# Kernel optimization log

Measured on AMD Instinct MI355X. Metric: run time of the kernel, lower is better.

Reference implementation:

```python
import jax, jax.numpy as jnp
import numpy as np

B, D, SLOTS, TOPK, CODE, ANCH = 8192, 64, 32, 3, 128, 32
BETA = 0.25  # vq_commitment_beta


def _clinear(zr, zi, Wr, Wi, br, bi):
    # ComplexLinear: real = Wr(zr)-Wi(zi), imag = Wi(zr)+Wr(zi); each nn.Linear carries its own bias
    return (zr @ Wr + br) - (zi @ Wi + bi), (zr @ Wi + bi) + (zi @ Wr + br)


def _layernorm(x, g, b, eps=1e-6):
    m = x.mean(-1, keepdims=True)
    v = ((x - m) ** 2).mean(-1, keepdims=True)  # biased var, as torch LayerNorm
    return (x - m) / jnp.sqrt(v + eps) * g + b


def setup_inputs() -> dict:
    key = jax.random.key(0)
    ks = jax.random.split(key, 16)
    f = jax.random.normal
    s = 0.05
    rng_init = 1.0 / np.sqrt(D)
    return dict(
        curr_r=f(ks[0], (B, D)), curr_i=f(ks[1], (B, D)),
        mem_r=f(ks[2], (B, SLOTS, D)), mem_i=f(ks[3], (B, SLOTS, D)),
        codebook=jax.random.uniform(ks[4], (CODE, 2 * D), minval=-rng_init, maxval=rng_init),
        qkv_Wr=f(ks[5], (3, D, D)) * s, qkv_Wi=f(ks[6], (3, D, D)) * s,
        qkv_br=jnp.zeros((3, D)), qkv_bi=jnp.zeros((3, D)),
        quad_Wr=f(ks[7], (D, D)) * s, quad_Wi=f(ks[8], (D, D)) * s,
        quad_br=jnp.zeros((D,)), quad_bi=jnp.zeros((D,)),
        sens_Wr=f(ks[9], (D, D)) * s, sens_Wi=f(ks[10], (D, D)) * s,
        sens_br=jnp.zeros((D,)), sens_bi=jnp.zeros((D,)),
        vis_palette=f(ks[11], (ANCH, 2 * D)), aud_palette=f(ks[12], (ANCH, 2 * D)),
        gate_W=f(ks[13], (2 * D, 1)) * s, gate_b=jnp.zeros((1,)),
        addr_W=f(ks[14], (2 * D, SLOTS)) * s, addr_b=jnp.zeros((SLOTS,)),
        ln_gamma_r=jnp.ones((D,)), ln_beta_r=jnp.zeros((D,)),
        ln_gamma_i=jnp.ones((D,)), ln_beta_i=jnp.zeros((D,)),
    )


def reference(curr_r, curr_i, mem_r, mem_i, codebook,
              qkv_Wr, qkv_Wi, qkv_br, qkv_bi,
              quad_Wr, quad_Wi, quad_br, quad_bi,
              sens_Wr, sens_Wi, sens_br, sens_bi,
              vis_palette, aud_palette,
              gate_W, gate_b, addr_W, addr_b,
              ln_gamma_r, ln_beta_r, ln_gamma_i, ln_beta_i):
    sg = jax.lax.stop_gradient
    z_flat = jnp.concatenate([curr_r, curr_i], -1)  # [B,2D]

    # ---- EMA_VQ (eval path): argmin codebook lookup + straight-through ----
    d = (z_flat ** 2).sum(1, keepdims=True) + (codebook ** 2).sum(1) - 2.0 * z_flat @ codebook.T
    d = jnp.maximum(d, 0.0)
    indices = jnp.argmin(d, -1)                      # [B]
    z_q = codebook[indices]                          # [B,2D]
    vq_loss = BETA * ((sg(z_q) - z_flat) ** 2).mean(-1)
    z_q = z_flat + sg(z_q - z_flat)
    probs = jnp.zeros((CODE,), z_flat.dtype).at[indices].add(1.0) / B
    norm_entropy = -(probs * jnp.log(probs + 1e-10)).sum() / np.log(CODE)
    vq_r, vq_i = z_q[..., :D], z_q[..., D:]

    # ---- HermitianGating ----
    qr, qi = _clinear(curr_r, curr_i, qkv_Wr[0], qkv_Wi[0], qkv_br[0], qkv_bi[0])
    kr, ki = _clinear(curr_r, curr_i, qkv_Wr[1], qkv_Wi[1], qkv_br[1], qkv_bi[1])
    vr, vi = _clinear(curr_r, curr_i, qkv_Wr[2], qkv_Wi[2], qkv_br[2], qkv_bi[2])
    gate = jax.nn.sigmoid((qr * kr + qi * ki).sum(-1, keepdims=True))
    g_r, g_i = vr * gate, vi * gate

    # ---- AssociativeMemory: softmax read + topk scatter write ----
    sim = jnp.einsum('bsd,bd->bs', mem_r, curr_r) + jnp.einsum('bsd,bd->bs', mem_i, curr_i)
    sim = sim - sg(sim.max(-1, keepdims=True))
    attn = jax.nn.softmax(sim, -1)
    read_r = jnp.einsum('bs,bsd->bd', attn, mem_r)
    read_i = jnp.einsum('bs,bsd->bd', attn, mem_i)
    write_gate = jax.nn.sigmoid(z_flat @ gate_W + gate_b)[:, :, None]  # [B,1,1]
    logits = z_flat @ addr_W + addr_b
    logits = logits - sg(logits.max(-1, keepdims=True))
    ww = jax.nn.softmax(logits, -1)                  # [B,SLOTS]
    slot_entropy = (-(ww * jnp.log(ww + 1e-10)).sum(-1)).mean()
    top_vals, top_idx = jax.lax.top_k(ww, TOPK)
    sparse = jnp.zeros_like(ww).at[jnp.arange(B)[:, None], top_idx].set(top_vals)
    sparse = sparse / (sparse.sum(-1, keepdims=True) + 1e-6)
    eff = write_gate * sparse[..., None]             # [B,SLOTS,1]
    nm_r = jnp.tanh(mem_r + eff * (curr_r[:, None, :] - mem_r))
    nm_i = jnp.tanh(mem_i + eff * (curr_i[:, None, :] - mem_i))
    nm_r = _layernorm(nm_r, ln_gamma_r, ln_beta_r)
    nm_i = _layernorm(nm_i, ln_gamma_i, ln_beta_i)

    # ---- SubmodalityAnchorModule ----
    s_r, s_i = _clinear(curr_r, curr_i, sens_Wr, sens_Wi, sens_br, sens_bi)
    sflat = jnp.concatenate([s_r, s_i], -1)

    def attend(pal):
        sc = sflat @ pal.T
        sc = sc - sg(sc.max(-1, keepdims=True))
        return jax.nn.softmax(sc, -1) @ pal

    vis = attend(vis_palette)
    aud = attend(aud_palette)
    exp_r = vis[..., :D] - aud[..., D:]   # vis_c + i*aud_c
    exp_i = vis[..., D:] + aud[..., :D]

    # ---- QuadratureModule: multiply by i ----
    zr, zi = _clinear(curr_r, curr_i, quad_Wr, quad_Wi, quad_br, quad_bi)
    q_r, q_i = -zi, zr

    combined = jnp.concatenate(
        [vq_r, vq_i, g_r, g_i, read_r, read_i, exp_r, exp_i, q_r, q_i,
         nm_r.reshape(B, -1), nm_i.reshape(B, -1)], -1)  # [B, 10*D + 2*SLOTS*D]
    return combined, vq_loss, indices, slot_entropy, norm_entropy
```

## Files before the change

### kernel.cpp

```cpp
#include <hip/hip_runtime.h>
#include <hip/hip_bf16.h>


#define NROWS 8
#define RSTRIDE 4736

static constexpr size_t OFF_VQLOSS = 38797312UL;
static constexpr size_t OFF_IDX    = 38805504UL;
static constexpr size_t OFF_SENT   = 38813696UL;
static constexpr size_t OFF_NENT   = 38813697UL;

struct Params {
  const float* curr_r; const float* curr_i;
  const float* mem_r;  const float* mem_i;
  const float* codebook;
  const float* qkv_Wr; const float* qkv_Wi; const float* qkv_br; const float* qkv_bi;
  const float* quad_Wr; const float* quad_Wi; const float* quad_br; const float* quad_bi;
  const float* sens_Wr; const float* sens_Wi; const float* sens_br; const float* sens_bi;
  const float* vis_pal; const float* aud_pal;
  const float* gate_W; const float* gate_b;
  const float* addr_W; const float* addr_b;
  const float* ln_gr; const float* ln_br; const float* ln_gi; const float* ln_bi;
  float* out;
  int* hist;
  float* rowent;
};

__device__ __forceinline__ float ftanh(float x) {
  const float e = __expf(2.0f * x);
  return 1.0f - 2.0f / (e + 1.0f);
}
__device__ __forceinline__ float fsigm(float x) {
  return 1.0f / (1.0f + __expf(-x));
}

union __align__(16) SharedU {
  struct {
    float zr[64], zi[64];
    float s_qr[64], s_qi[64], s_kr[64], s_ki[64], s_vr[64], s_vi[64];
    float sfl[128];
    float s_sp[4][4][64];
    float lp[4][32];
    float s_eff[32];
    float s_sim[32], s_attn[32];
    float s_rr[4][8][8], s_ri[4][8][8];
    float s_pv[4][32], s_pa[4][32];
    float s_pvp[32], s_pap[32];
    float s_vo[128], s_ao[128];
    float s_wg, s_gate;
  } r;
  struct {
    float s_zr[NROWS][64], s_zi[NROWS][64];
    double s_cbn[128];
    double s_dall4[4][256];
    float s_vqls[NROWS];
    int s_idx[NROWS];
  } v;
};

__global__ __launch_bounds__(256) void main_kernel(Params P) {
  __shared__ SharedU u;
  const int t = threadIdx.x;
  const int lane = t & 63;
  const int wv = t >> 6;

  if (blockIdx.x < 1024) {
    const int bid = blockIdx.x;
    {
      const float* cr = P.curr_r + (size_t)bid * (NROWS * 64);
      const float* ci = P.curr_i + (size_t)bid * (NROWS * 64);
      float* zr = &u.v.s_zr[0][0];
      float* zi = &u.v.s_zi[0][0];
      for (int i = t; i < NROWS * 64; i += 256) { zr[i] = cr[i]; zi[i] = ci[i]; }
    }
    {
      const float* cb = P.codebook + (t & 127) * 128 + (t >> 7) * 64;
      double a = 0.0;
      for (int d = 0; d < 64; ++d) { double w = (double)cb[d]; a = fma(w, w, a); }
      __syncthreads();
      ((double*)&u.v.s_dall4[0][0])[t] = a;
      __syncthreads();
      if (t < 128) u.v.s_cbn[t] = ((double*)&u.v.s_dall4[0][0])[t]
                                 + ((double*)&u.v.s_dall4[0][0])[t + 128];
      __syncthreads();
    }
    {
      const int c = t & 127, h = t >> 7;
      const float* cb = P.codebook + c * 128 + h * 64;
      const float (*zb)[64] = h ? u.v.s_zi : u.v.s_zr;
      #pragma unroll 1
      for (int p = 0; p < 2; ++p) {
        double acc[4];
        #pragma unroll
        for (int rr = 0; rr < 4; ++rr) acc[rr] = 0.0;
        for (int d = 0; d < 64; ++d) {
          const double w = (double)cb[d];
          #pragma unroll
          for (int rr = 0; rr < 4; ++rr) acc[rr] = fma(w, (double)zb[p * 4 + rr][d], acc[rr]);
        }
        #pragma unroll
        for (int rr = 0; rr < 4; ++rr) u.v.s_dall4[rr][h * 128 + c] = acc[rr];
        __syncthreads();
        {
          const int r = p * 4 + wv;
          const double d0 = u.v.s_cbn[lane]      - 2.0 * (u.v.s_dall4[wv][lane]      + u.v.s_dall4[wv][128 + lane]);
          const double d1 = u.v.s_cbn[lane + 64] - 2.0 * (u.v.s_dall4[wv][64 + lane] + u.v.s_dall4[wv][192 + lane]);
          double sv = d0; int si = lane;
          if (d1 < sv) { sv = d1; si = lane + 64; }
          #pragma unroll
          for (int m = 1; m <= 32; m <<= 1) {
            double ov = __shfl_xor(sv, m);
            int oi = __shfl_xor(si, m);
            if (ov < sv || (ov == sv && oi < si)) { sv = ov; si = oi; }
          }
          if (lane == 0) { u.v.s_idx[r] = si; atomicAdd(&P.hist[si], 1); }
        }
        __syncthreads();
      }
    }
    {
      #pragma unroll
      for (int rr = 0; rr < 2; ++rr) {
        const int r = wv * 2 + rr;
        const float* cb = P.codebook + (size_t)u.v.s_idx[r] * 128;
        float d0_ = cb[lane] - u.v.s_zr[r][lane];
        float d1_ = cb[64 + lane] - u.v.s_zi[r][lane];
        float v = d0_ * d0_ + d1_ * d1_;
        #pragma unroll
        for (int m = 1; m <= 32; m <<= 1) v += __shfl_xor(v, m);
        if (lane == 0) u.v.s_vqls[r] = 0.25f * v * (1.0f / 128.0f);
      }
    }
    __syncthreads();
    {
      const int j = t & 63, g = t >> 6;
      #pragma unroll
      for (int rr = 0; rr < 4; ++rr) {
        const int r = (g >> 1) * 4 + rr;
        float* orow = P.out + ((size_t)bid * NROWS + r) * RSTRIDE;
        const float* cb = P.codebook + (size_t)u.v.s_idx[r] * 128;
        if ((g & 1) == 0) {
          float z = u.v.s_zr[r][j];
          orow[j] = z + (cb[j] - z);
        } else {
          float z = u.v.s_zi[r][j];
          orow[64 + j] = z + (cb[64 + j] - z);
        }
      }
    }
    if (t < NROWS) {
      P.out[OFF_VQLOSS + (size_t)bid * NROWS + t] = u.v.s_vqls[t];
      P.out[OFF_IDX + (size_t)bid * NROWS + t] = (float)u.v.s_idx[t];
    }
    return;
  }

  const int b = blockIdx.x - 1024;
  const size_t bb = (size_t)b;
  const int s = t >> 3, k = t & 7, d0 = k * 8;
  const float* mrp = P.mem_r + ((bb * 32 + s) * 64 + d0);
  const float* mip = P.mem_i + ((bb * 32 + s) * 64 + d0);
  float4 a0 = *(const float4*)mrp, a1 = *(const float4*)(mrp + 4);
  float4 b0 = *(const float4*)mip, b1 = *(const float4*)(mip + 4);
  float mr[8] = {a0.x, a0.y, a0.z, a0.w, a1.x, a1.y, a1.z, a1.w};
  float mi[8] = {b0.x, b0.y, b0.z, b0.w, b1.x, b1.y, b1.z, b1.w};

  if (t < 64)       u.r.zr[t]      = P.curr_r[bb * 64 + t];
  else if (t < 128) u.r.zi[t - 64] = P.curr_i[bb * 64 + (t - 64)];
  __syncthreads();

  float* orow = P.out + bb * RSTRIDE;

  {
    const int j = lane, cl = wv;
    const float *Wr, *Wi, *br_, *bi_;
    if      (cl == 0) { Wr = P.qkv_Wr;        Wi = P.qkv_Wi;        br_ = P.qkv_br;       bi_ = P.qkv_bi;       }
    else if (cl == 1) { Wr = P.qkv_Wr + 4096; Wi = P.qkv_Wi + 4096; br_ = P.qkv_br + 64;  bi_ = P.qkv_bi + 64;  }
    else if (cl == 2) { Wr = P.qkv_Wr + 8192; Wi = P.qkv_Wi + 8192; br_ = P.qkv_br + 128; bi_ = P.qkv_bi + 128; }
    else              { Wr = P.quad_Wr;       Wi = P.quad_Wi;       br_ = P.quad_br;      bi_ = P.quad_bi;      }
    float aRR = 0.f, aRI = 0.f, aIR = 0.f, aII = 0.f;
    for (int d = 0; d < 64; ++d) {
      const float xr = u.r.zr[d], xi = u.r.zi[d];
      const float wr = Wr[d * 64 + j], wi = Wi[d * 64 + j];
      aRR += xr * wr; aRI += xr * wi; aIR += xi * wr; aII += xi * wi;
    }
    const float oR = (aRR + br_[j]) - (aII + bi_[j]);
    const float oI = (aRI + bi_[j]) + (aIR + br_[j]);
    if      (cl == 0) { u.r.s_qr[j] = oR; u.r.s_qi[j] = oI; }
    else if (cl == 1) { u.r.s_kr[j] = oR; u.r.s_ki[j] = oI; }
    else if (cl == 2) { u.r.s_vr[j] = oR; u.r.s_vi[j] = oI; }
    else              { orow[512 + j] = -oI; orow[576 + j] = oR; }
    float bRR = 0.f, bRI = 0.f, bIR = 0.f, bII = 0.f;
    for (int dd = 0; dd < 16; ++dd) {
      const int d = wv * 16 + dd;
      const float xr = u.r.zr[d], xi = u.r.zi[d];
      const float wr = P.sens_Wr[d * 64 + j], wi = P.sens_Wi[d * 64 + j];
      bRR += xr * wr; bRI += xr * wi; bIR += xi * wr; bII += xi * wi;
    }
    u.r.s_sp[wv][0][j] = bRR; u.r.s_sp[wv][1][j] = bRI;
    u.r.s_sp[wv][2][j] = bIR; u.r.s_sp[wv][3][j] = bII;
  }
  __syncthreads();

  {
    float sp = 0.f;
    #pragma unroll
    for (int x = 0; x < 8; ++x) sp += mr[x] * u.r.zr[d0 + x] + mi[x] * u.r.zi[d0 + x];
    sp += __shfl_xor(sp, 1); sp += __shfl_xor(sp, 2); sp += __shfl_xor(sp, 4);
    if (k == 0) u.r.s_sim[s] = sp;
  }
  if (t < 128) {
    const int q = t >> 5, l = t & 31;
    const float* zz = (q < 2) ? u.r.zr : u.r.zi;
    const int zb = (q & 1) * 32;
    float a = 0.f;
    for (int i = 0; i < 32; ++i) a += zz[zb + i] * P.addr_W[(q * 32 + i) * 32 + l];
    u.r.lp[q][l] = a;
  } else if (t < 192) {
    const int j = t - 128;
    float tw = u.r.zr[j] * P.gate_W[j] + u.r.zi[j] * P.gate_W[64 + j];
    #pragma unroll
    for (int m = 1; m <= 32; m <<= 1) tw += __shfl_xor(tw, m);
    if (j == 0) u.r.s_wg = tw;
  } else {
    const int j = t - 192;
    float g = u.r.s_qr[j] * u.r.s_kr[j] + u.r.s_qi[j] * u.r.s_ki[j];
    #pragma unroll
    for (int m = 1; m <= 32; m <<= 1) g += __shfl_xor(g, m);
    if (j == 0) u.r.s_gate = fsigm(g);
  }
  __syncthreads();

  if (t < 32) {
    float v = u.r.s_sim[t];
    float mx = v;
    #pragma unroll
    for (int m = 16; m >= 1; m >>= 1) mx = fmaxf(mx, __shfl_xor(mx, m));
    float e = __expf(v - mx);
    float sm = e;
    #pragma unroll
    for (int m = 16; m >= 1; m >>= 1) sm += __shfl_xor(sm, m);
    u.r.s_attn[t] = e / sm;
  } else if (t >= 64 && t < 96) {
    const int l = t - 64;
    float lg = u.r.lp[0][l] + u.r.lp[1][l] + u.r.lp[2][l] + u.r.lp[3][l] + P.addr_b[l];
    float mx = lg;
    #pragma unroll
    for (int m = 16; m >= 1; m >>= 1) mx = fmaxf(mx, __shfl_xor(mx, m));
    float e = __expf(lg - mx);
    float sm = e;
    #pragma unroll
    for (int m = 16; m >= 1; m >>= 1) sm += __shfl_xor(sm, m);
    const float w = e / sm;
    float es = -(w * __logf(w + 1e-10f));
    #pragma unroll
    for (int m = 16; m >= 1; m >>= 1) es += __shfl_xor(es, m);
    if (l == 0) P.rowent[b] = es;
    const float myw = w;
    bool picked = false;
    float val = w; int idx = l;
    float sumtop = 0.f;
    #pragma unroll
    for (int it = 0; it < 3; ++it) {
      float v2 = val; int i2 = idx;
      #pragma unroll
      for (int m = 16; m >= 1; m >>= 1) {
        float ov = __shfl_xor(v2, m); int oi = __shfl_xor(i2, m);
        if (ov > v2 || (ov == v2 && oi < i2)) { v2 = ov; i2 = oi; }
      }
      sumtop += v2;
      if (l == i2) { picked = true; val = -1e30f; }
    }
    const float wgate = fsigm(u.r.s_wg + P.gate_b[0]);
    u.r.s_eff[l] = picked ? wgate * (myw / (sumtop + 1e-6f)) : 0.f;
  } else if (t >= 128 && t < 192) {
    const int j = t - 128;
    const float aRR = u.r.s_sp[0][0][j] + u.r.s_sp[1][0][j] + u.r.s_sp[2][0][j] + u.r.s_sp[3][0][j];
    const float aRI = u.r.s_sp[0][1][j] + u.r.s_sp[1][1][j] + u.r.s_sp[2][1][j] + u.r.s_sp[3][1][j];
    const float aIR = u.r.s_sp[0][2][j] + u.r.s_sp[1][2][j] + u.r.s_sp[2][2][j] + u.r.s_sp[3][2][j];
    const float aII = u.r.s_sp[0][3][j] + u.r.s_sp[1][3][j] + u.r.s_sp[2][3][j] + u.r.s_sp[3][3][j];
    const float oR = (aRR + P.sens_br[j]) - (aII + P.sens_bi[j]);
    const float oI = (aRI + P.sens_bi[j]) + (aIR + P.sens_br[j]);
    u.r.sfl[j] = oR; u.r.sfl[64 + j] = oI;
  }
  __syncthreads();

  const float aw = u.r.s_attn[s];
  {
    float pr[8], pi[8];
    #pragma unroll
    for (int x = 0; x < 8; ++x) { pr[x] = aw * mr[x]; pi[x] = aw * mi[x]; }
    #pragma unroll
    for (int m = 8; m <= 32; m <<= 1) {
      #pragma unroll
      for (int x = 0; x < 8; ++x) { pr[x] += __shfl_xor(pr[x], m); pi[x] += __shfl_xor(pi[x], m); }
    }
    if (lane < 8) {
      #pragma unroll
      for (int x = 0; x < 8; ++x) { u.r.s_rr[wv][lane][x] = pr[x]; u.r.s_ri[wv][lane][x] = pi[x]; }
    }
  }
  {
    const float eff = u.r.s_eff[s];
    float nr[8], ni[8];
    #pragma unroll
    for (int x = 0; x < 8; ++x) {
      nr[x] = ftanh(mr[x] + eff * (u.r.zr[d0 + x] - mr[x]));
      ni[x] = ftanh(mi[x] + eff * (u.r.zi[d0 + x] - mi[x]));
    }
    float sR = 0.f, sI = 0.f;
    #pragma unroll
    for (int x = 0; x < 8; ++x) { sR += nr[x]; sI += ni[x]; }
    sR += __shfl_xor(sR, 1); sR += __shfl_xor(sR, 2); sR += __shfl_xor(sR, 4);
    sI += __shfl_xor(sI, 1); sI += __shfl_xor(sI, 2); sI += __shfl_xor(sI, 4);
    const float mR = sR * (1.f / 64.f), mI = sI * (1.f / 64.f);
    float vR = 0.f, vI = 0.f;
    #pragma unroll
    for (int x = 0; x < 8; ++x) {
      const float dr = nr[x] - mR; vR += dr * dr;
      const float di = ni[x] - mI; vI += di * di;
    }
    vR += __shfl_xor(vR, 1); vR += __shfl_xor(vR, 2); vR += __shfl_xor(vR, 4);
    vI += __shfl_xor(vI, 1); vI += __shfl_xor(vI, 2); vI += __shfl_xor(vI, 4);
    const float invR = 1.f / sqrtf(vR * (1.f / 64.f) + 1e-6f);
    const float invI = 1.f / sqrtf(vI * (1.f / 64.f) + 1e-6f);
    float oR[8], oI[8];
    #pragma unroll
    for (int x = 0; x < 8; ++x) {
      const int d = d0 + x;
      oR[x] = (nr[x] - mR) * invR * P.ln_gr[d] + P.ln_br[d];
      oI[x] = (ni[x] - mI) * invI * P.ln_gi[d] + P.ln_bi[d];
    }
    *(float4*)&orow[640 + s * 64 + d0]      = make_float4(oR[0], oR[1], oR[2], oR[3]);
    *(float4*)&orow[640 + s * 64 + d0 + 4]  = make_float4(oR[4], oR[5], oR[6], oR[7]);
    *(float4*)&orow[2688 + s * 64 + d0]     = make_float4(oI[0], oI[1], oI[2], oI[3]);
    *(float4*)&orow[2688 + s * 64 + d0 + 4] = make_float4(oI[4], oI[5], oI[6], oI[7]);
  }
  if (t < 128) {
    const int a = t & 31, q = t >> 5;
    float sc = 0.f;
    for (int x = q * 32; x < q * 32 + 32; ++x) sc += u.r.sfl[x] * P.vis_pal[a * 128 + x];
    u.r.s_pv[q][a] = sc;
  } else {
    const int tt = t - 128, a = tt & 31, q = tt >> 5;
    float sc = 0.f;
    for (int x = q * 32; x < q * 32 + 32; ++x) sc += u.r.sfl[x] * P.aud_pal[a * 128 + x];
    u.r.s_pa[q][a] = sc;
  }
  __syncthreads();

  if (t < 64) {
    const int kk = t >> 3, xx = t & 7;
    const float rv = u.r.s_rr[0][kk][xx] + u.r.s_rr[1][kk][xx] + u.r.s_rr[2][kk][xx] + u.r.s_rr[3][kk][xx];
    const float iv = u.r.s_ri[0][kk][xx] + u.r.s_ri[1][kk][xx] + u.r.s_ri[2][kk][xx] + u.r.s_ri[3][kk][xx];
    orow[256 + t] = rv;
    orow[320 + t] = iv;
  } else if (t >= 128 && t < 160) {
    const int a = t - 128;
    float sc = u.r.s_pv[0][a] + u.r.s_pv[1][a] + u.r.s_pv[2][a] + u.r.s_pv[3][a];
    float mx = sc;
    #pragma unroll
    for (int m = 16; m >= 1; m >>= 1) mx = fmaxf(mx, __shfl_xor(mx, m));
    float e = __expf(sc - mx);
    float sm = e;
    #pragma unroll
    for (int m = 16; m >= 1; m >>= 1) sm += __shfl_xor(sm, m);
    u.r.s_pvp[a] = e / sm;
  } else if (t >= 192 && t < 224) {
    const int a = t - 192;
    float sc = u.r.s_pa[0][a] + u.r.s_pa[1][a] + u.r.s_pa[2][a] + u.r.s_pa[3][a];
    float mx = sc;
    #pragma unroll
    for (int m = 16; m >= 1; m >>= 1) mx = fmaxf(mx, __shfl_xor(mx, m));
    float e = __expf(sc - mx);
    float sm = e;
    #pragma unroll
    for (int m = 16; m >= 1; m >>= 1) sm += __shfl_xor(sm, m);
    u.r.s_pap[a] = e / sm;
  }
  __syncthreads();

  if (t < 128) {
    float v = 0.f;
    for (int a = 0; a < 32; ++a) v += u.r.s_pvp[a] * P.vis_pal[a * 128 + t];
    u.r.s_vo[t] = v;
  } else {
    const int j = t - 128;
    float v = 0.f;
    for (int a = 0; a < 32; ++a) v += u.r.s_pap[a] * P.aud_pal[a * 128 + j];
    u.r.s_ao[j] = v;
  }
  if (t < 64)       orow[128 + t] = u.r.s_vr[t] * u.r.s_gate;
  else if (t < 128) orow[192 + (t - 64)] = u.r.s_vi[t - 64] * u.r.s_gate;
  __syncthreads();

  if (t < 64)       orow[384 + t] = u.r.s_vo[t] - u.r.s_ao[64 + t];
  else if (t < 128) orow[448 + (t - 64)] = u.r.s_vo[t] + u.r.s_ao[t - 64];
}

__global__ __launch_bounds__(256) void finalize_k(const int* hist, const float* rowent,
                                                  float* out) {
  const int t = threadIdx.x;
  __shared__ float red[256];
  float se = 0.f;
  for (int i = t; i < 8192; i += 256) se += rowent[i];
  red[t] = se;
  __syncthreads();
  for (int off = 128; off >= 1; off >>= 1) {
    if (t < off) red[t] += red[t + off];
    __syncthreads();
  }
  if (t == 0) out[OFF_SENT] = red[0] / 8192.0f;
  __syncthreads();
  float ne = 0.f;
  if (t < 128) {
    const float pp = (float)hist[t] / 8192.0f;
    ne = -(pp * logf(pp + 1e-10f));
  }
  red[t] = ne;
  __syncthreads();
  for (int off = 128; off >= 1; off >>= 1) {
    if (t < off) red[t] += red[t + off];
    __syncthreads();
  }
  if (t == 0) out[OFF_NENT] = red[0] / logf(128.0f);
}

extern "C" void kernel_launch(void* const* d_in, const int* in_sizes, int n_in,
                              void* d_out, int out_size, void* d_ws, size_t ws_size,
                              hipStream_t stream) {
  (void)in_sizes; (void)n_in; (void)out_size; (void)ws_size;
  Params P;
  P.curr_r   = (const float*)d_in[0];
  P.curr_i   = (const float*)d_in[1];
  P.mem_r    = (const float*)d_in[2];
  P.mem_i    = (const float*)d_in[3];
  P.codebook = (const float*)d_in[4];
  P.qkv_Wr   = (const float*)d_in[5];
  P.qkv_Wi   = (const float*)d_in[6];
  P.qkv_br   = (const float*)d_in[7];
  P.qkv_bi   = (const float*)d_in[8];
  P.quad_Wr  = (const float*)d_in[9];
  P.quad_Wi  = (const float*)d_in[10];
  P.quad_br  = (const float*)d_in[11];
  P.quad_bi  = (const float*)d_in[12];
  P.sens_Wr  = (const float*)d_in[13];
  P.sens_Wi  = (const float*)d_in[14];
  P.sens_br  = (const float*)d_in[15];
  P.sens_bi  = (const float*)d_in[16];
  P.vis_pal  = (const float*)d_in[17];
  P.aud_pal  = (const float*)d_in[18];
  P.gate_W   = (const float*)d_in[19];
  P.gate_b   = (const float*)d_in[20];
  P.addr_W   = (const float*)d_in[21];
  P.addr_b   = (const float*)d_in[22];
  P.ln_gr    = (const float*)d_in[23];
  P.ln_br    = (const float*)d_in[24];
  P.ln_gi    = (const float*)d_in[25];
  P.ln_bi    = (const float*)d_in[26];
  P.out = (float*)d_out;
  P.hist = (int*)d_ws;
  P.rowent = (float*)((char*)d_ws + 512);

  hipMemsetAsync(d_ws, 0, 512, stream);
  main_kernel<<<dim3(1024 + 8192), dim3(256), 0, stream>>>(P);
  finalize_k<<<dim3(1), dim3(256), 0, stream>>>(P.hist, P.rowent, (float*)d_out);
}
```

Before: 234.4 us.

## Process four batch rows per block with register prefetch of next row

Each per-row block now loops over four consecutive batch rows, and the grid shrinks from 8192 row blocks to 2048. While computing the current row, it prefetches the next row's memory slots and current vector into registers, so global load latency overlaps with compute. Weight reads from cache are shared across rows. In exchange each block runs longer, there are fewer blocks to spread over the GPU, an extra barrier is added per row, and register pressure rises.

```diff
diff --git a/kernel.cpp b/kernel.cpp
--- a/kernel.cpp
+++ b/kernel.cpp
@@ -155,247 +155,278 @@
     return;
   }
 
-  const int b = blockIdx.x - 1024;
-  const size_t bb = (size_t)b;
+  const int base = (blockIdx.x - 1024) * 4;
   const int s = t >> 3, k = t & 7, d0 = k * 8;
-  const float* mrp = P.mem_r + ((bb * 32 + s) * 64 + d0);
-  const float* mip = P.mem_i + ((bb * 32 + s) * 64 + d0);
-  float4 a0 = *(const float4*)mrp, a1 = *(const float4*)(mrp + 4);
-  float4 b0 = *(const float4*)mip, b1 = *(const float4*)(mip + 4);
-  float mr[8] = {a0.x, a0.y, a0.z, a0.w, a1.x, a1.y, a1.z, a1.w};
-  float mi[8] = {b0.x, b0.y, b0.z, b0.w, b1.x, b1.y, b1.z, b1.w};
-
-  if (t < 64)       u.r.zr[t]      = P.curr_r[bb * 64 + t];
-  else if (t < 128) u.r.zi[t - 64] = P.curr_i[bb * 64 + (t - 64)];
+
+  float mrC[8], miC[8], mrN[8], miN[8];
+  {
+    const size_t bb0 = (size_t)base;
+    const float* mrp = P.mem_r + ((bb0 * 32 + s) * 64 + d0);
+    const float* mip = P.mem_i + ((bb0 * 32 + s) * 64 + d0);
+    float4 a0 = *(const float4*)mrp, a1 = *(const float4*)(mrp + 4);
+    float4 b0 = *(const float4*)mip, b1 = *(const float4*)(mip + 4);
+    mrC[0]=a0.x; mrC[1]=a0.y; mrC[2]=a0.z; mrC[3]=a0.w; mrC[4]=a1.x; mrC[5]=a1.y; mrC[6]=a1.z; mrC[7]=a1.w;
+    miC[0]=b0.x; miC[1]=b0.y; miC[2]=b0.z; miC[3]=b0.w; miC[4]=b1.x; miC[5]=b1.y; miC[6]=b1.z; miC[7]=b1.w;
+    if (t < 64)       u.r.zr[t]      = P.curr_r[bb0 * 64 + t];
+    else if (t < 128) u.r.zi[t - 64] = P.curr_i[bb0 * 64 + (t - 64)];
+  }
   __syncthreads();
 
-  float* orow = P.out + bb * RSTRIDE;
-
-  {
-    const int j = lane, cl = wv;
-    const float *Wr, *Wi, *br_, *bi_;
-    if      (cl == 0) { Wr = P.qkv_Wr;        Wi = P.qkv_Wi;        br_ = P.qkv_br;       bi_ = P.qkv_bi;       }
-    else if (cl == 1) { Wr = P.qkv_Wr + 4096; Wi = P.qkv_Wi + 4096; br_ = P.qkv_br + 64;  bi_ = P.qkv_bi + 64;  }
-    else if (cl == 2) { Wr = P.qkv_Wr + 8192; Wi = P.qkv_Wi + 8192; br_ = P.qkv_br + 128; bi_ = P.qkv_bi + 128; }
-    else              { Wr = P.quad_Wr;       Wi = P.quad_Wi;       br_ = P.quad_br;      bi_ = P.quad_bi;      }
-    float aRR = 0.f, aRI = 0.f, aIR = 0.f, aII = 0.f;
-    for (int d = 0; d < 64; ++d) {
-      const float xr = u.r.zr[d], xi = u.r.zi[d];
-      const float wr = Wr[d * 64 + j], wi = Wi[d * 64 + j];
-      aRR += xr * wr; aRI += xr * wi; aIR += xi * wr; aII += xi * wi;
-    }
-    const float oR = (aRR + br_[j]) - (aII + bi_[j]);
-    const float oI = (aRI + bi_[j]) + (aIR + br_[j]);
-    if      (cl == 0) { u.r.s_qr[j] = oR; u.r.s_qi[j] = oI; }
-    else if (cl == 1) { u.r.s_kr[j] = oR; u.r.s_ki[j] = oI; }
-    else if (cl == 2) { u.r.s_vr[j] = oR; u.r.s_vi[j] = oI; }
-    else              { orow[512 + j] = -oI; orow[576 + j] = oR; }
-    float bRR = 0.f, bRI = 0.f, bIR = 0.f, bII = 0.f;
-    for (int dd = 0; dd < 16; ++dd) {
-      const int d = wv * 16 + dd;
-      const float xr = u.r.zr[d], xi = u.r.zi[d];
-      const float wr = P.sens_Wr[d * 64 + j], wi = P.sens_Wi[d * 64 + j];
-      bRR += xr * wr; bRI += xr * wi; bIR += xi * wr; bII += xi * wi;
-    }
-    u.r.s_sp[wv][0][j] = bRR; u.r.s_sp[wv][1][j] = bRI;
-    u.r.s_sp[wv][2][j] = bIR; u.r.s_sp[wv][3][j] = bII;
-  }
-  __syncthreads();
-
-  {
-    float sp = 0.f;
-    #pragma unroll
-    for (int x = 0; x < 8; ++x) sp += mr[x] * u.r.zr[d0 + x] + mi[x] * u.r.zi[d0 + x];
-    sp += __shfl_xor(sp, 1); sp += __shfl_xor(sp, 2); sp += __shfl_xor(sp, 4);
-    if (k == 0) u.r.s_sim[s] = sp;
-  }
-  if (t < 128) {
-    const int q = t >> 5, l = t & 31;
-    const float* zz = (q < 2) ? u.r.zr : u.r.zi;
-    const int zb = (q & 1) * 32;
-    float a = 0.f;
-    for (int i = 0; i < 32; ++i) a += zz[zb + i] * P.addr_W[(q * 32 + i) * 32 + l];
-    u.r.lp[q][l] = a;
-  } else if (t < 192) {
-    const int j = t - 128;
-    float tw = u.r.zr[j] * P.gate_W[j] + u.r.zi[j] * P.gate_W[64 + j];
-    #pragma unroll
-    for (int m = 1; m <= 32; m <<= 1) tw += __shfl_xor(tw, m);
-    if (j == 0) u.r.s_wg = tw;
-  } else {
-    const int j = t - 192;
-    float g = u.r.s_qr[j] * u.r.s_kr[j] + u.r.s_qi[j] * u.r.s_ki[j];
-    #pragma unroll
-    for (int m = 1; m <= 32; m <<= 1) g += __shfl_xor(g, m);
-    if (j == 0) u.r.s_gate = fsigm(g);
-  }
-  __syncthreads();
-
-  if (t < 32) {
-    float v = u.r.s_sim[t];
-    float mx = v;
-    #pragma unroll
-    for (int m = 16; m >= 1; m >>= 1) mx = fmaxf(mx, __shfl_xor(mx, m));
-    float e = __expf(v - mx);
-    float sm = e;
-    #pragma unroll
-    for (int m = 16; m >= 1; m >>= 1) sm += __shfl_xor(sm, m);
-    u.r.s_attn[t] = e / sm;
-  } else if (t >= 64 && t < 96) {
-    const int l = t - 64;
-    float lg = u.r.lp[0][l] + u.r.lp[1][l] + u.r.lp[2][l] + u.r.lp[3][l] + P.addr_b[l];
-    float mx = lg;
-    #pragma unroll
-    for (int m = 16; m >= 1; m >>= 1) mx = fmaxf(mx, __shfl_xor(mx, m));
-    float e = __expf(lg - mx);
-    float sm = e;
-    #pragma unroll
-    for (int m = 16; m >= 1; m >>= 1) sm += __shfl_xor(sm, m);
-    const float w = e / sm;
-    float es = -(w * __logf(w + 1e-10f));
-    #pragma unroll
-    for (int m = 16; m >= 1; m >>= 1) es += __shfl_xor(es, m);
-    if (l == 0) P.rowent[b] = es;
-    const float myw = w;
-    bool picked = false;
-    float val = w; int idx = l;
-    float sumtop = 0.f;
-    #pragma unroll
-    for (int it = 0; it < 3; ++it) {
-      float v2 = val; int i2 = idx;
-      #pragma unroll
-      for (int m = 16; m >= 1; m >>= 1) {
-        float ov = __shfl_xor(v2, m); int oi = __shfl_xor(i2, m);
-        if (ov > v2 || (ov == v2 && oi < i2)) { v2 = ov; i2 = oi; }
-      }
-      sumtop += v2;
-      if (l == i2) { picked = true; val = -1e30f; }
-    }
-    const float wgate = fsigm(u.r.s_wg + P.gate_b[0]);
-    u.r.s_eff[l] = picked ? wgate * (myw / (sumtop + 1e-6f)) : 0.f;
-  } else if (t >= 128 && t < 192) {
-    const int j = t - 128;
-    const float aRR = u.r.s_sp[0][0][j] + u.r.s_sp[1][0][j] + u.r.s_sp[2][0][j] + u.r.s_sp[3][0][j];
-    const float aRI = u.r.s_sp[0][1][j] + u.r.s_sp[1][1][j] + u.r.s_sp[2][1][j] + u.r.s_sp[3][1][j];
-    const float aIR = u.r.s_sp[0][2][j] + u.r.s_sp[1][2][j] + u.r.s_sp[2][2][j] + u.r.s_sp[3][2][j];
-    const float aII = u.r.s_sp[0][3][j] + u.r.s_sp[1][3][j] + u.r.s_sp[2][3][j] + u.r.s_sp[3][3][j];
-    const float oR = (aRR + P.sens_br[j]) - (aII + P.sens_bi[j]);
-    const float oI = (aRI + P.sens_bi[j]) + (aIR + P.sens_br[j]);
-    u.r.sfl[j] = oR; u.r.sfl[64 + j] = oI;
-  }
-  __syncthreads();
-
-  const float aw = u.r.s_attn[s];
-  {
-    float pr[8], pi[8];
-    #pragma unroll
-    for (int x = 0; x < 8; ++x) { pr[x] = aw * mr[x]; pi[x] = aw * mi[x]; }
-    #pragma unroll
-    for (int m = 8; m <= 32; m <<= 1) {
-      #pragma unroll
-      for (int x = 0; x < 8; ++x) { pr[x] += __shfl_xor(pr[x], m); pi[x] += __shfl_xor(pi[x], m); }
-    }
-    if (lane < 8) {
-      #pragma unroll
-      for (int x = 0; x < 8; ++x) { u.r.s_rr[wv][lane][x] = pr[x]; u.r.s_ri[wv][lane][x] = pi[x]; }
-    }
-  }
-  {
-    const float eff = u.r.s_eff[s];
-    float nr[8], ni[8];
-    #pragma unroll
-    for (int x = 0; x < 8; ++x) {
-      nr[x] = ftanh(mr[x] + eff * (u.r.zr[d0 + x] - mr[x]));
-      ni[x] = ftanh(mi[x] + eff * (u.r.zi[d0 + x] - mi[x]));
-    }
-    float sR = 0.f, sI = 0.f;
-    #pragma unroll
-    for (int x = 0; x < 8; ++x) { sR += nr[x]; sI += ni[x]; }
-    sR += __shfl_xor(sR, 1); sR += __shfl_xor(sR, 2); sR += __shfl_xor(sR, 4);
-    sI += __shfl_xor(sI, 1); sI += __shfl_xor(sI, 2); sI += __shfl_xor(sI, 4);
-    const float mR = sR * (1.f / 64.f), mI = sI * (1.f / 64.f);
-    float vR = 0.f, vI = 0.f;
-    #pragma unroll
-    for (int x = 0; x < 8; ++x) {
-      const float dr = nr[x] - mR; vR += dr * dr;
-      const float di = ni[x] - mI; vI += di * di;
-    }
-    vR += __shfl_xor(vR, 1); vR += __shfl_xor(vR, 2); vR += __shfl_xor(vR, 4);
-    vI += __shfl_xor(vI, 1); vI += __shfl_xor(vI, 2); vI += __shfl_xor(vI, 4);
-    const float invR = 1.f / sqrtf(vR * (1.f / 64.f) + 1e-6f);
-    const float invI = 1.f / sqrtf(vI * (1.f / 64.f) + 1e-6f);
-    float oR[8], oI[8];
-    #pragma unroll
-    for (int x = 0; x < 8; ++x) {
-      const int d = d0 + x;
-      oR[x] = (nr[x] - mR) * invR * P.ln_gr[d] + P.ln_br[d];
-      oI[x] = (ni[x] - mI) * invI * P.ln_gi[d] + P.ln_bi[d];
-    }
-    *(float4*)&orow[640 + s * 64 + d0]      = make_float4(oR[0], oR[1], oR[2], oR[3]);
-    *(float4*)&orow[640 + s * 64 + d0 + 4]  = make_float4(oR[4], oR[5], oR[6], oR[7]);
-    *(float4*)&orow[2688 + s * 64 + d0]     = make_float4(oI[0], oI[1], oI[2], oI[3]);
-    *(float4*)&orow[2688 + s * 64 + d0 + 4] = make_float4(oI[4], oI[5], oI[6], oI[7]);
-  }
-  if (t < 128) {
-    const int a = t & 31, q = t >> 5;
-    float sc = 0.f;
-    for (int x = q * 32; x < q * 32 + 32; ++x) sc += u.r.sfl[x] * P.vis_pal[a * 128 + x];
-    u.r.s_pv[q][a] = sc;
-  } else {
-    const int tt = t - 128, a = tt & 31, q = tt >> 5;
-    float sc = 0.f;
-    for (int x = q * 32; x < q * 32 + 32; ++x) sc += u.r.sfl[x] * P.aud_pal[a * 128 + x];
-    u.r.s_pa[q][a] = sc;
-  }
-  __syncthreads();
-
-  if (t < 64) {
-    const int kk = t >> 3, xx = t & 7;
-    const float rv = u.r.s_rr[0][kk][xx] + u.r.s_rr[1][kk][xx] + u.r.s_rr[2][kk][xx] + u.r.s_rr[3][kk][xx];
-    const float iv = u.r.s_ri[0][kk][xx] + u.r.s_ri[1][kk][xx] + u.r.s_ri[2][kk][xx] + u.r.s_ri[3][kk][xx];
-    orow[256 + t] = rv;
-    orow[320 + t] = iv;
-  } else if (t >= 128 && t < 160) {
-    const int a = t - 128;
-    float sc = u.r.s_pv[0][a] + u.r.s_pv[1][a] + u.r.s_pv[2][a] + u.r.s_pv[3][a];
-    float mx = sc;
-    #pragma unroll
-    for (int m = 16; m >= 1; m >>= 1) mx = fmaxf(mx, __shfl_xor(mx, m));
-    float e = __expf(sc - mx);
-    float sm = e;
-    #pragma unroll
-    for (int m = 16; m >= 1; m >>= 1) sm += __shfl_xor(sm, m);
-    u.r.s_pvp[a] = e / sm;
-  } else if (t >= 192 && t < 224) {
-    const int a = t - 192;
-    float sc = u.r.s_pa[0][a] + u.r.s_pa[1][a] + u.r.s_pa[2][a] + u.r.s_pa[3][a];
-    float mx = sc;
-    #pragma unroll
-    for (int m = 16; m >= 1; m >>= 1) mx = fmaxf(mx, __shfl_xor(mx, m));
-    float e = __expf(sc - mx);
-    float sm = e;
-    #pragma unroll
-    for (int m = 16; m >= 1; m >>= 1) sm += __shfl_xor(sm, m);
-    u.r.s_pap[a] = e / sm;
-  }
-  __syncthreads();
-
-  if (t < 128) {
-    float v = 0.f;
-    for (int a = 0; a < 32; ++a) v += u.r.s_pvp[a] * P.vis_pal[a * 128 + t];
-    u.r.s_vo[t] = v;
-  } else {
-    const int j = t - 128;
-    float v = 0.f;
-    for (int a = 0; a < 32; ++a) v += u.r.s_pap[a] * P.aud_pal[a * 128 + j];
-    u.r.s_ao[j] = v;
-  }
-  if (t < 64)       orow[128 + t] = u.r.s_vr[t] * u.r.s_gate;
-  else if (t < 128) orow[192 + (t - 64)] = u.r.s_vi[t - 64] * u.r.s_gate;
-  __syncthreads();
-
-  if (t < 64)       orow[384 + t] = u.r.s_vo[t] - u.r.s_ao[64 + t];
-  else if (t < 128) orow[448 + (t - 64)] = u.r.s_vo[t] + u.r.s_ao[t - 64];
+  #pragma unroll
+  for (int rr = 0; rr < 4; ++rr) {
+    const int b = base + rr;
+    const size_t bb = (size_t)b;
+    float* orow = P.out + bb * RSTRIDE;
+
+    float zn = 0.f;
+    if (rr < 3) {
+      const size_t bn = bb + 1;
+      const float* mrp = P.mem_r + ((bn * 32 + s) * 64 + d0);
+      const float* mip = P.mem_i + ((bn * 32 + s) * 64 + d0);
+      float4 a0 = *(const float4*)mrp, a1 = *(const float4*)(mrp + 4);
+      float4 b0 = *(const float4*)mip, b1 = *(const float4*)(mip + 4);
+      mrN[0]=a0.x; mrN[1]=a0.y; mrN[2]=a0.z; mrN[3]=a0.w; mrN[4]=a1.x; mrN[5]=a1.y; mrN[6]=a1.z; mrN[7]=a1.w;
+      miN[0]=b0.x; miN[1]=b0.y; miN[2]=b0.z; miN[3]=b0.w; miN[4]=b1.x; miN[5]=b1.y; miN[6]=b1.z; miN[7]=b1.w;
+      if (t < 64)       zn = P.curr_r[bn * 64 + t];
+      else if (t < 128) zn = P.curr_i[bn * 64 + (t - 64)];
+    }
+
+    {
+      const int j = lane, cl = wv;
+      const float *Wr, *Wi, *br_, *bi_;
+      if      (cl == 0) { Wr = P.qkv_Wr;        Wi = P.qkv_Wi;        br_ = P.qkv_br;       bi_ = P.qkv_bi;       }
+      else if (cl == 1) { Wr = P.qkv_Wr + 4096; Wi = P.qkv_Wi + 4096; br_ = P.qkv_br + 64;  bi_ = P.qkv_bi + 64;  }
+      else if (cl == 2) { Wr = P.qkv_Wr + 8192; Wi = P.qkv_Wi + 8192; br_ = P.qkv_br + 128; bi_ = P.qkv_bi + 128; }
+      else              { Wr = P.quad_Wr;       Wi = P.quad_Wi;       br_ = P.quad_br;      bi_ = P.quad_bi;      }
+      float aRR = 0.f, aRI = 0.f, aIR = 0.f, aII = 0.f;
+      for (int d = 0; d < 64; ++d) {
+        const float xr = u.r.zr[d], xi = u.r.zi[d];
+        const float wr = Wr[d * 64 + j], wi = Wi[d * 64 + j];
+        aRR += xr * wr; aRI += xr * wi; aIR += xi * wr; aII += xi * wi;
+      }
+      const float oR = (aRR + br_[j]) - (aII + bi_[j]);
+      const float oI = (aRI + bi_[j]) + (aIR + br_[j]);
+      if      (cl == 0) { u.r.s_qr[j] = oR; u.r.s_qi[j] = oI; }
+      else if (cl == 1) { u.r.s_kr[j] = oR; u.r.s_ki[j] = oI; }
+      else if (cl == 2) { u.r.s_vr[j] = oR; u.r.s_vi[j] = oI; }
+      else              { orow[512 + j] = -oI; orow[576 + j] = oR; }
+      float bRR = 0.f, bRI = 0.f, bIR = 0.f, bII = 0.f;
+      for (int dd = 0; dd < 16; ++dd) {
+        const int d = wv * 16 + dd;
+        const float xr = u.r.zr[d], xi = u.r.zi[d];
+        const float wr = P.sens_Wr[d * 64 + j], wi = P.sens_Wi[d * 64 + j];
+        bRR += xr * wr; bRI += xr * wi; bIR += xi * wr; bII += xi * wi;
+      }
+      u.r.s_sp[wv][0][j] = bRR; u.r.s_sp[wv][1][j] = bRI;
+      u.r.s_sp[wv][2][j] = bIR; u.r.s_sp[wv][3][j] = bII;
+    }
+    __syncthreads();
+
+    {
+      float sp = 0.f;
+      #pragma unroll
+      for (int x = 0; x < 8; ++x) sp += mrC[x] * u.r.zr[d0 + x] + miC[x] * u.r.zi[d0 + x];
+      sp += __shfl_xor(sp, 1); sp += __shfl_xor(sp, 2); sp += __shfl_xor(sp, 4);
+      if (k == 0) u.r.s_sim[s] = sp;
+    }
+    if (t < 128) {
+      const int q = t >> 5, l = t & 31;
+      const float* zz = (q < 2) ? u.r.zr : u.r.zi;
+      const int zb = (q & 1) * 32;
+      float a = 0.f;
+      for (int i = 0; i < 32; ++i) a += zz[zb + i] * P.addr_W[(q * 32 + i) * 32 + l];
+      u.r.lp[q][l] = a;
+    } else if (t < 192) {
+      const int j = t - 128;
+      float tw = u.r.zr[j] * P.gate_W[j] + u.r.zi[j] * P.gate_W[64 + j];
+      #pragma unroll
+      for (int m = 1; m <= 32; m <<= 1) tw += __shfl_xor(tw, m);
+      if (j == 0) u.r.s_wg = tw;
+    } else {
+      const int j = t - 192;
+      float g = u.r.s_qr[j] * u.r.s_kr[j] + u.r.s_qi[j] * u.r.s_ki[j];
+      #pragma unroll
+      for (int m = 1; m <= 32; m <<= 1) g += __shfl_xor(g, m);
+      if (j == 0) u.r.s_gate = fsigm(g);
+    }
+    __syncthreads();
+
+    if (t < 32) {
+      float v = u.r.s_sim[t];
+      float mx = v;
+      #pragma unroll
+      for (int m = 16; m >= 1; m >>= 1) mx = fmaxf(mx, __shfl_xor(mx, m));
+      float e = __expf(v - mx);
+      float sm = e;
+      #pragma unroll
+      for (int m = 16; m >= 1; m >>= 1) sm += __shfl_xor(sm, m);
+      u.r.s_attn[t] = e / sm;
+    } else if (t >= 64 && t < 96) {
+      const int l = t - 64;
+      float lg = u.r.lp[0][l] + u.r.lp[1][l] + u.r.lp[2][l] + u.r.lp[3][l] + P.addr_b[l];
+      float mx = lg;
+      #pragma unroll
+      for (int m = 16; m >= 1; m >>= 1) mx = fmaxf(mx, __shfl_xor(mx, m));
+      float e = __expf(lg - mx);
+      float sm = e;
+      #pragma unroll
+      for (int m = 16; m >= 1; m >>= 1) sm += __shfl_xor(sm, m);
+      const float w = e / sm;
+      float es = -(w * __logf(w + 1e-10f));
+      #pragma unroll
+      for (int m = 16; m >= 1; m >>= 1) es += __shfl_xor(es, m);
+      if (l == 0) P.rowent[b] = es;
+      const float myw = w;
+      bool picked = false;
+      float val = w; int idx = l;
+      float sumtop = 0.f;
+      #pragma unroll
+      for (int it = 0; it < 3; ++it) {
+        float v2 = val; int i2 = idx;
+        #pragma unroll
+        for (int m = 16; m >= 1; m >>= 1) {
+          float ov = __shfl_xor(v2, m); int oi = __shfl_xor(i2, m);
+          if (ov > v2 || (ov == v2 && oi < i2)) { v2 = ov; i2 = oi; }
+        }
+        sumtop += v2;
+        if (l == i2) { picked = true; val = -1e30f; }
+      }
+      const float wgate = fsigm(u.r.s_wg + P.gate_b[0]);
+      u.r.s_eff[l] = picked ? wgate * (myw / (sumtop + 1e-6f)) : 0.f;
+    } else if (t >= 128 && t < 192) {
+      const int j = t - 128;
+      const float aRR = u.r.s_sp[0][0][j] + u.r.s_sp[1][0][j] + u.r.s_sp[2][0][j] + u.r.s_sp[3][0][j];
+      const float aRI = u.r.s_sp[0][1][j] + u.r.s_sp[1][1][j] + u.r.s_sp[2][1][j] + u.r.s_sp[3][1][j];
+      const float aIR = u.r.s_sp[0][2][j] + u.r.s_sp[1][2][j] + u.r.s_sp[2][2][j] + u.r.s_sp[3][2][j];
+      const float aII = u.r.s_sp[0][3][j] + u.r.s_sp[1][3][j] + u.r.s_sp[2][3][j] + u.r.s_sp[3][3][j];
+      const float oR = (aRR + P.sens_br[j]) - (aII + P.sens_bi[j]);
+      const float oI = (aRI + P.sens_bi[j]) + (aIR + P.sens_br[j]);
+      u.r.sfl[j] = oR; u.r.sfl[64 + j] = oI;
+    }
+    __syncthreads();
+
+    const float aw = u.r.s_attn[s];
+    {
+      float pr[8], pi[8];
+      #pragma unroll
+      for (int x = 0; x < 8; ++x) { pr[x] = aw * mrC[x]; pi[x] = aw * miC[x]; }
+      #pragma unroll
+      for (int m = 8; m <= 32; m <<= 1) {
+        #pragma unroll
+        for (int x = 0; x < 8; ++x) { pr[x] += __shfl_xor(pr[x], m); pi[x] += __shfl_xor(pi[x], m); }
+      }
+      if (lane < 8) {
+        #pragma unroll
+        for (int x = 0; x < 8; ++x) { u.r.s_rr[wv][lane][x] = pr[x]; u.r.s_ri[wv][lane][x] = pi[x]; }
+      }
+    }
+    {
+      const float eff = u.r.s_eff[s];
+      float nr[8], ni[8];
+      #pragma unroll
+      for (int x = 0; x < 8; ++x) {
+        nr[x] = ftanh(mrC[x] + eff * (u.r.zr[d0 + x] - mrC[x]));
+        ni[x] = ftanh(miC[x] + eff * (u.r.zi[d0 + x] - miC[x]));
+      }
+      float sR = 0.f, sI = 0.f;
+      #pragma unroll
+      for (int x = 0; x < 8; ++x) { sR += nr[x]; sI += ni[x]; }
+      sR += __shfl_xor(sR, 1); sR += __shfl_xor(sR, 2); sR += __shfl_xor(sR, 4);
+      sI += __shfl_xor(sI, 1); sI += __shfl_xor(sI, 2); sI += __shfl_xor(sI, 4);
+      const float mR = sR * (1.f / 64.f), mI = sI * (1.f / 64.f);
+      float vR = 0.f, vI = 0.f;
+      #pragma unroll
+      for (int x = 0; x < 8; ++x) {
+        const float dr = nr[x] - mR; vR += dr * dr;
+        const float di = ni[x] - mI; vI += di * di;
+      }
+      vR += __shfl_xor(vR, 1); vR += __shfl_xor(vR, 2); vR += __shfl_xor(vR, 4);
+      vI += __shfl_xor(vI, 1); vI += __shfl_xor(vI, 2); vI += __shfl_xor(vI, 4);
+      const float invR = 1.f / sqrtf(vR * (1.f / 64.f) + 1e-6f);
+      const float invI = 1.f / sqrtf(vI * (1.f / 64.f) + 1e-6f);
+      float oR[8], oI[8];
+      #pragma unroll
+      for (int x = 0; x < 8; ++x) {
+        const int d = d0 + x;
+        oR[x] = (nr[x] - mR) * invR * P.ln_gr[d] + P.ln_br[d];
+        oI[x] = (ni[x] - mI) * invI * P.ln_gi[d] + P.ln_bi[d];
+      }
+      *(float4*)&orow[640 + s * 64 + d0]      = make_float4(oR[0], oR[1], oR[2], oR[3]);
+      *(float4*)&orow[640 + s * 64 + d0 + 4]  = make_float4(oR[4], oR[5], oR[6], oR[7]);
+      *(float4*)&orow[2688 + s * 64 + d0]     = make_float4(oI[0], oI[1], oI[2], oI[3]);
+      *(float4*)&orow[2688 + s * 64 + d0 + 4] = make_float4(oI[4], oI[5], oI[6], oI[7]);
+    }
+    if (t < 128) {
+      const int a = t & 31, q = t >> 5;
+      float sc = 0.f;
+      for (int x = q * 32; x < q * 32 + 32; ++x) sc += u.r.sfl[x] * P.vis_pal[a * 128 + x];
+      u.r.s_pv[q][a] = sc;
+    } else {
+      const int tt = t - 128, a = tt & 31, q = tt >> 5;
+      float sc = 0.f;
+      for (int x = q * 32; x < q * 32 + 32; ++x) sc += u.r.sfl[x] * P.aud_pal[a * 128 + x];
+      u.r.s_pa[q][a] = sc;
+    }
+    __syncthreads();
+
+    if (rr < 3 && t < 128) {
+      if (t < 64) u.r.zr[t] = zn;
+      else        u.r.zi[t - 64] = zn;
+    }
+    if (t < 64) {
+      const int kk = t >> 3, xx = t & 7;
+      const float rv = u.r.s_rr[0][kk][xx] + u.r.s_rr[1][kk][xx] + u.r.s_rr[2][kk][xx] + u.r.s_rr[3][kk][xx];
+      const float iv = u.r.s_ri[0][kk][xx] + u.r.s_ri[1][kk][xx] + u.r.s_ri[2][kk][xx] + u.r.s_ri[3][kk][xx];
+      orow[256 + t] = rv;
+      orow[320 + t] = iv;
+    } else if (t >= 128 && t < 160) {
+      const int a = t - 128;
+      float sc = u.r.s_pv[0][a] + u.r.s_pv[1][a] + u.r.s_pv[2][a] + u.r.s_pv[3][a];
+      float mx = sc;
+      #pragma unroll
+      for (int m = 16; m >= 1; m >>= 1) mx = fmaxf(mx, __shfl_xor(mx, m));
+      float e = __expf(sc - mx);
+      float sm = e;
+      #pragma unroll
+      for (int m = 16; m >= 1; m >>= 1) sm += __shfl_xor(sm, m);
+      u.r.s_pvp[a] = e / sm;
+    } else if (t >= 192 && t < 224) {
+      const int a = t - 192;
+      float sc = u.r.s_pa[0][a] + u.r.s_pa[1][a] + u.r.s_pa[2][a] + u.r.s_pa[3][a];
+      float mx = sc;
+      #pragma unroll
+      for (int m = 16; m >= 1; m >>= 1) mx = fmaxf(mx, __shfl_xor(mx, m));
+      float e = __expf(sc - mx);
+      float sm = e;
+      #pragma unroll
+      for (int m = 16; m >= 1; m >>= 1) sm += __shfl_xor(sm, m);
+      u.r.s_pap[a] = e / sm;
+    }
+    __syncthreads();
+
+    if (t < 128) {
+      float v = 0.f;
+      for (int a = 0; a < 32; ++a) v += u.r.s_pvp[a] * P.vis_pal[a * 128 + t];
+      u.r.s_vo[t] = v;
+    } else {
+      const int j = t - 128;
+      float v = 0.f;
+      for (int a = 0; a < 32; ++a) v += u.r.s_pap[a] * P.aud_pal[a * 128 + j];
+      u.r.s_ao[j] = v;
+    }
+    if (t < 64)       orow[128 + t] = u.r.s_vr[t] * u.r.s_gate;
+    else if (t < 128) orow[192 + (t - 64)] = u.r.s_vi[t - 64] * u.r.s_gate;
+    __syncthreads();
+
+    if (t < 64)       orow[384 + t] = u.r.s_vo[t] - u.r.s_ao[64 + t];
+    else if (t < 128) orow[448 + (t - 64)] = u.r.s_vo[t] + u.r.s_ao[t - 64];
+    __syncthreads();
+
+    if (rr < 3) {
+      #pragma unroll
+      for (int x = 0; x < 8; ++x) { mrC[x] = mrN[x]; miC[x] = miN[x]; }
+    }
+  }
 }
 
 __global__ __launch_bounds__(256) void finalize_k(const int* hist, const float* rowent,
@@ -463,6 +494,6 @@
   P.rowent = (float*)((char*)d_ws + 512);
 
   hipMemsetAsync(d_ws, 0, 512, stream);
-  main_kernel<<<dim3(1024 + 8192), dim3(256), 0, stream>>>(P);
+  main_kernel<<<dim3(1024 + 2048), dim3(256), 0, stream>>>(P);
   finalize_k<<<dim3(1), dim3(256), 0, stream>>>(P.hist, P.rowent, (float*)d_out);
 }
```

Measured after the change: 637.2 us. 2.72x slower.
